# Kernel tuning notes

Hardware: AMD Instinct MI355X
Metric: run time of the kernel (lower is better)

## Reference

```python
import jax, jax.numpy as jnp
import numpy as np

HIDDEN = 4096
INTER = 14336
TOKENS = 4096


def setup_inputs() -> dict:
    key = jax.random.key(0)
    k_x, k_g, k_u, k_d = jax.random.split(key, 4)
    scale_in = 1.0 / np.sqrt(HIDDEN)
    scale_mid = 1.0 / np.sqrt(INTER)
    return {
        "x": jax.random.normal(k_x, (TOKENS, HIDDEN), dtype=jnp.float32),
        "w_gate": jax.random.normal(k_g, (HIDDEN, INTER), dtype=jnp.float32) * scale_in,
        "w_up": jax.random.normal(k_u, (HIDDEN, INTER), dtype=jnp.float32) * scale_in,
        "w_down": jax.random.normal(k_d, (INTER, HIDDEN), dtype=jnp.float32) * scale_mid,
    }


def reference(x, w_gate, w_up, w_down):
    # SwiGLU: down( silu(x @ Wg) * (x @ Wu) )
    gate = jax.nn.silu(jnp.einsum("td,df->tf", x, w_gate))  # [T, INTER]
    up = jnp.einsum("td,df->tf", x, w_up)                   # [T, INTER]
    return jnp.einsum("tf,fd->td", gate * up, w_down)       # [T, HIDDEN]
```

## Files before the change

### kernel.cpp

```cpp
#include <hip/hip_runtime.h>

#define H_DIM 4096
#define I_DIM 14336
#define T_DIM 4096
#define N2    (2*I_DIM)

typedef float  f32x4  __attribute__((ext_vector_type(4)));
typedef float  f32x2  __attribute__((ext_vector_type(2)));
typedef unsigned int u32x4 __attribute__((ext_vector_type(4)));
typedef unsigned int u32x2 __attribute__((ext_vector_type(2)));
typedef __bf16 bf16x8 __attribute__((ext_vector_type(8)));
typedef unsigned short u16;

__device__ __forceinline__ unsigned int pack2bf(float a, float b){
  unsigned int ua = __builtin_bit_cast(unsigned int, a);
  unsigned int ub = __builtin_bit_cast(unsigned int, b);
  ua = (ua + 0x7fffu + ((ua >> 16) & 1u)) >> 16;
  ub = (ub + 0x7fffu + ((ub >> 16) & 1u)) >> 16;
  return (ua & 0xffffu) | (ub << 16);
}
__device__ __forceinline__ u16 f2bf(float a){
  unsigned int u = __builtin_bit_cast(unsigned int, a);
  u = (u + 0x7fffu + ((u >> 16) & 1u)) >> 16;
  return (u16)u;
}
__device__ __forceinline__ bf16x8 lds_frag(const unsigned char* p){
  u32x4 v = *(const u32x4*)p;
  return __builtin_bit_cast(bf16x8, v);
}

#define GLOAD16(g, l) __builtin_amdgcn_global_load_lds( \
    (const __attribute__((address_space(1))) unsigned int*)(g), \
    (__attribute__((address_space(3))) unsigned int*)(l), 16, 0, 0)

#define WAITVM0  asm volatile("s_waitcnt vmcnt(0)" ::: "memory")
#define CFENCE   asm volatile("" ::: "memory")

__global__ __launch_bounds__(256)
void k_cast(const float* __restrict__ in, u16* __restrict__ out, long n)
{
  long i = ((long)blockIdx.x * 256 + threadIdx.x) * 8;
  if (i >= n) return;
  f32x4 a = *(const f32x4*)(in + i);
  f32x4 b = *(const f32x4*)(in + i + 4);
  u32x4 o = { pack2bf(a[0],a[1]), pack2bf(a[2],a[3]),
              pack2bf(b[0],b[1]), pack2bf(b[2],b[3]) };
  *(u32x4*)(out + i) = o;
}

__global__ __launch_bounds__(256)
void k_transpose(const float* __restrict__ in, u16* __restrict__ out,
                 int R, int C, int remap)
{
  __shared__ u16 tile[64][68];
  const int tid = threadIdx.x;
  const int r0 = blockIdx.x * 64, c0 = blockIdx.y * 64;
  const int lr  = tid >> 4;
  const int lc4 = (tid & 15) * 4;
  #pragma unroll
  for (int s = 0; s < 4; ++s){
    f32x4 v = *(const f32x4*)(in + (size_t)(r0 + lr + s*16) * C + c0 + lc4);
    #pragma unroll
    for (int j = 0; j < 4; ++j) tile[lc4 + j][lr + s*16] = f2bf(v[j]);
  }
  __syncthreads();
  #pragma unroll
  for (int s = 0; s < 4; ++s){
    int cl = lr + s*16;
    int n  = c0 + cl;
    int orow = (remap < 0) ? n : (((n >> 4) << 5) + (n & 15) + remap);
    u32x2 v = *(const u32x2*)&tile[cl][lc4];
    *(u32x2*)(out + (size_t)orow * R + r0 + lc4) = v;
  }
}

template<int EPI>
__global__ __launch_bounds__(512, 2)
void gemm9(const u16* __restrict__ A, const u16* __restrict__ B,
           void* __restrict__ Cout, const int K, const int ldc,
           const int mblocks)
{
  __shared__ unsigned char smem[131072];
  const int tid  = threadIdx.x;
  const int lane = tid & 63;
  const int wid  = tid >> 6;
  const int wm   = wid >> 2;
  const int wn   = wid & 3;

  const int nwg = gridDim.x;
  const int cpx = nwg >> 3;
  const int bid = blockIdx.x;
  const int swz = (bid & 7) * cpx + (bid >> 3);
  const int m0 = (swz % mblocks) << 8;
  const int n0 = (swz / mblocks) << 8;
  const int NT = K >> 6;

  const int srow = tid >> 3;
  const int gl   = (tid & 7) ^ (srow & 7);
  const u16* Ap = A + (size_t)(m0 + srow) * K + gl * 8;
  const u16* Bp = B + (size_t)(n0 + srow) * K + gl * 8;
  unsigned char* ldsw = smem + tid * 16;
  const size_t rowK64  = (size_t)64 * K;
  const size_t rowK128 = (size_t)128 * K;

  const int r15 = lane & 15;
  const int lhi = lane >> 4;
  const int gk0 = (((r15 >> 2) & 1) << 2) | (lhi ^ (r15 & 3));
  const int gk1 = gk0 ^ 4;
  const unsigned char* ldsr = smem + r15 * 128;

  f32x4 acc[8][4];
  #pragma unroll
  for (int i = 0; i < 8; ++i)
    #pragma unroll
    for (int j = 0; j < 4; ++j) acc[i][j] = (f32x4)0.0f;
  bf16x8 areg0[4][2], areg1[4][2];
  bf16x8 breg[2][2][2];

#define ISSUE(h) do { \
    const int _a = (h) & 3; \
    const size_t _k0 = (size_t)((h) >> 2) << 6; \
    unsigned char* _l = ldsw + (((h) & 7) << 14); \
    const u16* _s = (_a < 2 ? Bp + (size_t)_a * rowK128 \
                            : Ap + (size_t)(_a - 2) * rowK128) + _k0; \
    GLOAD16(_s, _l); \
    GLOAD16(_s + rowK64, _l + 8192); \
  } while (0)

#define RD_A(SLOT, MQ, DST) do { \
    const unsigned char* _b = ldsr + ((SLOT) << 14) + (MQ) * 8192; \
    _Pragma("unroll") \
    for (int _m = 0; _m < 4; ++_m) { \
      DST[_m][0] = lds_frag(_b + _m * 2048 + gk0 * 16); \
      DST[_m][1] = lds_frag(_b + _m * 2048 + gk1 * 16); \
    } \
  } while (0)

#define RD_B(SLOT, NQ) do { \
    const unsigned char* _b = ldsr + ((SLOT) << 14) + (wn & 1) * 8192 + (NQ) * 4096; \
    _Pragma("unroll") \
    for (int _n = 0; _n < 2; ++_n) { \
      breg[NQ][_n][0] = lds_frag(_b + _n * 2048 + gk0 * 16); \
      breg[NQ][_n][1] = lds_frag(_b + _n * 2048 + gk1 * 16); \
    } \
  } while (0)

#define MFMAQ(AR, MQ, NQ) \
    _Pragma("unroll") \
    for (int _m = 0; _m < 4; ++_m) \
      _Pragma("unroll") \
      for (int _n = 0; _n < 2; ++_n) { \
        acc[(MQ)*4+_m][(NQ)*2+_n] = __builtin_amdgcn_mfma_f32_16x16x32_bf16( \
            AR[_m][0], breg[NQ][_n][0], acc[(MQ)*4+_m][(NQ)*2+_n], 0, 0, 0); \
        acc[(MQ)*4+_m][(NQ)*2+_n] = __builtin_amdgcn_mfma_f32_16x16x32_bf16( \
            AR[_m][1], breg[NQ][_n][1], acc[(MQ)*4+_m][(NQ)*2+_n], 0, 0, 0); \
      }

  #pragma unroll
  for (int h = 0; h < 4; ++h) ISSUE(h);
  WAITVM0;
  __builtin_amdgcn_s_barrier();
  CFENCE;

  for (int t = 0; t < NT; ++t){
    const int bh = t << 2;
    const int sB = (bh + (wn >> 1)) & 7;
    const int sA = (bh + 2 + wm) & 7;
    const bool more = (t + 1 < NT);
    if (more){ ISSUE(bh + 4); ISSUE(bh + 5); ISSUE(bh + 6); ISSUE(bh + 7); }
    RD_A(sA, 0, areg0);
    RD_B(sB, 0);
    RD_B(sB, 1);
    MFMAQ(areg0, 0, 0);
    RD_A(sA, 1, areg1);
    MFMAQ(areg0, 0, 1);
    MFMAQ(areg1, 1, 1);
    MFMAQ(areg1, 1, 0);
    if (more) WAITVM0;
    __builtin_amdgcn_s_barrier();
    CFENCE;
  }

#undef ISSUE
#undef RD_A
#undef RD_B
#undef MFMAQ

  const int r0 = lhi * 4;
  if (EPI == 0){
    float* C = (float*)Cout;
    #pragma unroll
    for (int mi = 0; mi < 8; ++mi)
      #pragma unroll
      for (int nj = 0; nj < 4; ++nj)
        #pragma unroll
        for (int j = 0; j < 4; ++j)
          C[(size_t)(m0 + wm*128 + mi*16 + r0 + j) * ldc + n0 + wn*64 + nj*16 + r15] =
            acc[mi][nj][j];
  } else {
    u16* C = (u16*)Cout;
    const int hb = ((n0 + wn*64) >> 1);
    #pragma unroll
    for (int mi = 0; mi < 8; ++mi)
      #pragma unroll
      for (int p = 0; p < 2; ++p)
        #pragma unroll
        for (int j = 0; j < 4; ++j){
          float g = acc[mi][2*p][j];
          float u = acc[mi][2*p+1][j];
          float s = g / (1.0f + __expf(-g));
          C[(size_t)(m0 + wm*128 + mi*16 + r0 + j) * ldc + hb + p*16 + r15] =
            f2bf(s * u);
        }
  }
}

__global__ __launch_bounds__(256, 2)
void k_gateup_fb(const float* __restrict__ x, const float* __restrict__ wg,
                 const float* __restrict__ wu, u16* __restrict__ h)
{
  __shared__ unsigned char smem[61440];
  const int tid  = threadIdx.x;
  const int lane = tid & 63;
  const int wid  = tid >> 6;
  const int wr   = wid >> 1, wc = wid & 1;
  const int m0   = blockIdx.x * 128;
  const int n0   = blockIdx.y * 128;
  const int s_am = tid >> 3;
  const int s_ak = (tid & 7) * 4;
  const int s_bn = (tid & 63) * 2;
  const int s_bk = (tid >> 6) * 8;

  f32x4 accg[4][4], accu[4][4];
  #pragma unroll
  for (int i = 0; i < 4; ++i)
    #pragma unroll
    for (int j = 0; j < 4; ++j){ accg[i][j] = (f32x4)0.0f; accu[i][j] = (f32x4)0.0f; }

  f32x4 pa[4];
  f32x2 pg[8], pu[8];
  auto gload = [&](int kt){
    const int k0 = kt * 32;
    #pragma unroll
    for (int it = 0; it < 4; ++it)
      pa[it] = *(const f32x4*)(x + (size_t)(m0 + it*32 + s_am) * H_DIM + k0 + s_ak);
    #pragma unroll
    for (int r = 0; r < 8; ++r){
      pg[r] = *(const f32x2*)(wg + (size_t)(k0 + s_bk + r) * I_DIM + n0 + s_bn);
      pu[r] = *(const f32x2*)(wu + (size_t)(k0 + s_bk + r) * I_DIM + n0 + s_bn);
    }
  };
  auto sstore = [&](int b){
    unsigned char* Ab = smem + b * 10240;
    #pragma unroll
    for (int it = 0; it < 4; ++it){
      u32x2 v = { pack2bf(pa[it][0], pa[it][1]), pack2bf(pa[it][2], pa[it][3]) };
      *(u32x2*)(Ab + (s_am + it*32) * 80 + s_ak * 2) = v;
    }
    unsigned char* Bg = smem + 20480 + b * 10240;
    unsigned char* Bu = smem + 40960 + b * 10240;
    #pragma unroll
    for (int c = 0; c < 2; ++c){
      u32x4 vg = { pack2bf(pg[0][c], pg[1][c]), pack2bf(pg[2][c], pg[3][c]),
                   pack2bf(pg[4][c], pg[5][c]), pack2bf(pg[6][c], pg[7][c]) };
      *(u32x4*)(Bg + (s_bn + c) * 80 + s_bk * 2) = vg;
      u32x4 vu = { pack2bf(pu[0][c], pu[1][c]), pack2bf(pu[2][c], pu[3][c]),
                   pack2bf(pu[4][c], pu[5][c]), pack2bf(pu[6][c], pu[7][c]) };
      *(u32x4*)(Bu + (s_bn + c) * 80 + s_bk * 2) = vu;
    }
  };
  const int koff = (lane >> 4) * 16;
  const int ar   = wr * 64 + (lane & 15);
  const int br   = wc * 64 + (lane & 15);
  auto compute = [&](int b){
    const unsigned char* Ab = smem + b * 10240;
    const unsigned char* Bg = smem + 20480 + b * 10240;
    const unsigned char* Bu = smem + 40960 + b * 10240;
    bf16x8 a[4];
    #pragma unroll
    for (int mi = 0; mi < 4; ++mi)
      a[mi] = lds_frag(Ab + (ar + mi*16) * 80 + koff);
    #pragma unroll
    for (int nh = 0; nh < 2; ++nh){
      bf16x8 bg[2], bu[2];
      #pragma unroll
      for (int nj = 0; nj < 2; ++nj){
        bg[nj] = lds_frag(Bg + (br + (nh*2+nj)*16) * 80 + koff);
        bu[nj] = lds_frag(Bu + (br + (nh*2+nj)*16) * 80 + koff);
      }
      #pragma unroll
      for (int mi = 0; mi < 4; ++mi)
        #pragma unroll
        for (int nj = 0; nj < 2; ++nj){
          accg[mi][nh*2+nj] = __builtin_amdgcn_mfma_f32_16x16x32_bf16(a[mi], bg[nj], accg[mi][nh*2+nj], 0, 0, 0);
          accu[mi][nh*2+nj] = __builtin_amdgcn_mfma_f32_16x16x32_bf16(a[mi], bu[nj], accu[mi][nh*2+nj], 0, 0, 0);
        }
    }
  };
  gload(0); sstore(0); __syncthreads();
  const int NT = H_DIM / 32;
  for (int kt = 0; kt < NT; ++kt){
    const int b = kt & 1;
    if (kt + 1 < NT) gload(kt + 1);
    compute(b);
    if (kt + 1 < NT) sstore(b ^ 1);
    __syncthreads();
  }
  const int bm = wr * 64 + ((lane >> 4) << 2);
  const int bn = wc * 64 + (lane & 15);
  #pragma unroll
  for (int mi = 0; mi < 4; ++mi)
    #pragma unroll
    for (int ni = 0; ni < 4; ++ni)
      #pragma unroll
      for (int r = 0; r < 4; ++r){
        float gv = accg[mi][ni][r];
        float uv = accu[mi][ni][r];
        float s  = gv / (1.0f + __expf(-gv));
        h[(size_t)(m0 + bm + mi*16 + r) * I_DIM + n0 + bn + ni*16] = f2bf(s * uv);
      }
}

__global__ __launch_bounds__(256, 2)
void k_down_fb(const u16* __restrict__ h, const float* __restrict__ wd,
               float* __restrict__ out)
{
  __shared__ unsigned char smem[40960];
  const int tid  = threadIdx.x;
  const int lane = tid & 63;
  const int wid  = tid >> 6;
  const int wr   = wid >> 1, wc = wid & 1;
  const int m0   = blockIdx.x * 128;
  const int n0   = blockIdx.y * 128;
  const int s_am = tid >> 1;
  const int s_ak = (tid & 1) * 16;
  const int s_bn = (tid & 63) * 2;
  const int s_bk = (tid >> 6) * 8;

  f32x4 acc[4][4];
  #pragma unroll
  for (int i = 0; i < 4; ++i)
    #pragma unroll
    for (int j = 0; j < 4; ++j) acc[i][j] = (f32x4)0.0f;

  u32x4 pha[2];
  f32x2 pb[8];
  auto gload = [&](int kt){
    const int k0 = kt * 32;
    const u16* ap = h + (size_t)(m0 + s_am) * I_DIM + k0 + s_ak;
    pha[0] = *(const u32x4*)(ap);
    pha[1] = *(const u32x4*)(ap + 8);
    #pragma unroll
    for (int r = 0; r < 8; ++r)
      pb[r] = *(const f32x2*)(wd + (size_t)(k0 + s_bk + r) * H_DIM + n0 + s_bn);
  };
  auto sstore = [&](int b){
    unsigned char* Ab = smem + b * 10240;
    *(u32x4*)(Ab + s_am * 80 + s_ak * 2)      = pha[0];
    *(u32x4*)(Ab + s_am * 80 + s_ak * 2 + 16) = pha[1];
    unsigned char* Bb = smem + 20480 + b * 10240;
    #pragma unroll
    for (int c = 0; c < 2; ++c){
      u32x4 v = { pack2bf(pb[0][c], pb[1][c]), pack2bf(pb[2][c], pb[3][c]),
                  pack2bf(pb[4][c], pb[5][c]), pack2bf(pb[6][c], pb[7][c]) };
      *(u32x4*)(Bb + (s_bn + c) * 80 + s_bk * 2) = v;
    }
  };
  const int koff = (lane >> 4) * 16;
  const int ar   = wr * 64 + (lane & 15);
  const int br   = wc * 64 + (lane & 15);
  auto compute = [&](int b){
    const unsigned char* Ab = smem + b * 10240;
    const unsigned char* Bb = smem + 20480 + b * 10240;
    bf16x8 a[4];
    #pragma unroll
    for (int mi = 0; mi < 4; ++mi)
      a[mi] = lds_frag(Ab + (ar + mi*16) * 80 + koff);
    #pragma unroll
    for (int nh = 0; nh < 2; ++nh){
      bf16x8 bb[2];
      #pragma unroll
      for (int nj = 0; nj < 2; ++nj)
        bb[nj] = lds_frag(Bb + (br + (nh*2+nj)*16) * 80 + koff);
      #pragma unroll
      for (int mi = 0; mi < 4; ++mi)
        #pragma unroll
        for (int nj = 0; nj < 2; ++nj)
          acc[mi][nh*2+nj] = __builtin_amdgcn_mfma_f32_16x16x32_bf16(a[mi], bb[nj], acc[mi][nh*2+nj], 0, 0, 0);
    }
  };
  gload(0); sstore(0); __syncthreads();
  const int NT = I_DIM / 32;
  for (int kt = 0; kt < NT; ++kt){
    const int b = kt & 1;
    if (kt + 1 < NT) gload(kt + 1);
    compute(b);
    if (kt + 1 < NT) sstore(b ^ 1);
    __syncthreads();
  }
  const int bm = wr * 64 + ((lane >> 4) << 2);
  const int bn = wc * 64 + (lane & 15);
  #pragma unroll
  for (int mi = 0; mi < 4; ++mi)
    #pragma unroll
    for (int ni = 0; ni < 4; ++ni)
      #pragma unroll
      for (int r = 0; r < 4; ++r)
        out[(size_t)(m0 + bm + mi*16 + r) * H_DIM + n0 + bn + ni*16] = acc[mi][ni][r];
}

extern "C" void kernel_launch(void* const* d_in, const int* in_sizes, int n_in,
                              void* d_out, int out_size, void* d_ws, size_t ws_size,
                              hipStream_t stream)
{
  const float* x  = (const float*)d_in[0];
  const float* wg = (const float*)d_in[1];
  const float* wu = (const float*)d_in[2];
  const float* wd = (const float*)d_in[3];
  float* out = (float*)d_out;

  const size_t X_OFF   = 0;
  const size_t WGU_OFF = 33554432;
  const size_t WD_OFF  = 268435456;
  const size_t H_OFF   = 385875968;
  const size_t NEED    = 503316480;

  if (ws_size >= NEED){
    u16* xb  = (u16*)((char*)d_ws + X_OFF);
    u16* wgu = (u16*)((char*)d_ws + WGU_OFF);
    u16* wdt = (u16*)((char*)d_ws + WD_OFF);
    u16* h   = (u16*)((char*)d_ws + H_OFF);

    long nx = (long)T_DIM * H_DIM;
    k_cast<<<(unsigned)((nx/8 + 255)/256), 256, 0, stream>>>(x, xb, nx);
    dim3 tg(H_DIM/64, I_DIM/64);
    k_transpose<<<tg, 256, 0, stream>>>(wg, wgu, H_DIM, I_DIM, 0);
    k_transpose<<<tg, 256, 0, stream>>>(wu, wgu, H_DIM, I_DIM, 16);
    dim3 td(I_DIM/64, H_DIM/64);
    k_transpose<<<td, 256, 0, stream>>>(wd, wdt, I_DIM, H_DIM, -1);

    gemm9<1><<<dim3(16 * (N2/256)), dim3(512), 0, stream>>>(
        xb, wgu, h, H_DIM, I_DIM, T_DIM/256);
    gemm9<0><<<dim3(16 * (H_DIM/256)), dim3(512), 0, stream>>>(
        h, wdt, out, I_DIM, H_DIM, T_DIM/256);
  } else {
    u16* h = (u16*)d_ws;
    size_t maxrows = ws_size / ((size_t)I_DIM * 2);
    int chunk = (int)(maxrows > (size_t)T_DIM ? (size_t)T_DIM : maxrows);
    chunk &= ~127;
    if (chunk < 128) chunk = 128;
    for (int r0 = 0; r0 < T_DIM; r0 += chunk){
      int rows = (T_DIM - r0 < chunk) ? (T_DIM - r0) : chunk;
      dim3 g1(rows / 128, I_DIM / 128);
      dim3 g2(rows / 128, H_DIM / 128);
      k_gateup_fb<<<g1, dim3(256), 0, stream>>>(x + (size_t)r0 * H_DIM, wg, wu, h);
      k_down_fb  <<<g2, dim3(256), 0, stream>>>(h, wd, out + (size_t)r0 * H_DIM);
    }
  }
}
```

Measured before the change: 1.421 ms.

## Spread global-to-LDS prefetch across k-loop phases with finer barriers and priority

The GEMM main loop now issues one prefetch chunk per compute phase, staying six half-tiles ahead, instead of issuing four chunks at the top of each iteration and then waiting on all loads. It waits with vmcnt(4) instead of vmcnt(0) and adds a workgroup barrier between MFMA phases. MFMA sections are wrapped in s_setprio to favour the math waves. This is meant to keep loads in flight across iterations and hide memory latency, at the cost of three extra barriers per iteration and correctness depending on the ring-buffer slot reuse timing.

```diff
diff --git a/kernel.cpp b/kernel.cpp
--- a/kernel.cpp
+++ b/kernel.cpp
@@ -33,6 +33,7 @@
     (const __attribute__((address_space(1))) unsigned int*)(g), \
     (__attribute__((address_space(3))) unsigned int*)(l), 16, 0, 0)
 
+#define WAITVM4  asm volatile("s_waitcnt vmcnt(4)" ::: "memory")
 #define WAITVM0  asm volatile("s_waitcnt vmcnt(0)" ::: "memory")
 #define CFENCE   asm volatile("" ::: "memory")
 
@@ -76,9 +77,9 @@
 
 template<int EPI>
 __global__ __launch_bounds__(512, 2)
-void gemm9(const u16* __restrict__ A, const u16* __restrict__ B,
-           void* __restrict__ Cout, const int K, const int ldc,
-           const int mblocks)
+void gemm10(const u16* __restrict__ A, const u16* __restrict__ B,
+            void* __restrict__ Cout, const int K, const int ldc,
+            const int mblocks)
 {
   __shared__ unsigned char smem[131072];
   const int tid  = threadIdx.x;
@@ -157,8 +158,8 @@
       }
 
   #pragma unroll
-  for (int h = 0; h < 4; ++h) ISSUE(h);
-  WAITVM0;
+  for (int h = 0; h < 6; ++h) ISSUE(h);
+  WAITVM4;
   __builtin_amdgcn_s_barrier();
   CFENCE;
 
@@ -166,17 +167,34 @@
     const int bh = t << 2;
     const int sB = (bh + (wn >> 1)) & 7;
     const int sA = (bh + 2 + wm) & 7;
-    const bool more = (t + 1 < NT);
-    if (more){ ISSUE(bh + 4); ISSUE(bh + 5); ISSUE(bh + 6); ISSUE(bh + 7); }
+    const int lim = NT << 2;
     RD_A(sA, 0, areg0);
     RD_B(sB, 0);
+    if (bh + 6 < lim) ISSUE(bh + 6);
+    __builtin_amdgcn_s_setprio(1);
+    MFMAQ(areg0, 0, 0);
+    __builtin_amdgcn_s_setprio(0);
+    __builtin_amdgcn_s_barrier();
+    CFENCE;
     RD_B(sB, 1);
-    MFMAQ(areg0, 0, 0);
+    if (bh + 7 < lim) ISSUE(bh + 7);
+    __builtin_amdgcn_s_setprio(1);
+    MFMAQ(areg0, 0, 1);
+    __builtin_amdgcn_s_setprio(0);
+    __builtin_amdgcn_s_barrier();
+    CFENCE;
     RD_A(sA, 1, areg1);
-    MFMAQ(areg0, 0, 1);
+    if (bh + 8 < lim) ISSUE(bh + 8);
+    __builtin_amdgcn_s_setprio(1);
     MFMAQ(areg1, 1, 1);
+    __builtin_amdgcn_s_setprio(0);
+    __builtin_amdgcn_s_barrier();
+    CFENCE;
+    if (bh + 9 < lim) ISSUE(bh + 9);
+    __builtin_amdgcn_s_setprio(1);
     MFMAQ(areg1, 1, 0);
-    if (more) WAITVM0;
+    __builtin_amdgcn_s_setprio(0);
+    if (t + 2 < NT) { WAITVM4; } else { WAITVM0; }
     __builtin_amdgcn_s_barrier();
     CFENCE;
   }
@@ -439,9 +457,9 @@
     dim3 td(I_DIM/64, H_DIM/64);
     k_transpose<<<td, 256, 0, stream>>>(wd, wdt, I_DIM, H_DIM, -1);
 
-    gemm9<1><<<dim3(16 * (N2/256)), dim3(512), 0, stream>>>(
+    gemm10<1><<<dim3(16 * (N2/256)), dim3(512), 0, stream>>>(
         xb, wgu, h, H_DIM, I_DIM, T_DIM/256);
-    gemm9<0><<<dim3(16 * (H_DIM/256)), dim3(512), 0, stream>>>(
+    gemm10<0><<<dim3(16 * (H_DIM/256)), dim3(512), 0, stream>>>(
         h, wdt, out, I_DIM, H_DIM, T_DIM/256);
   } else {
     u16* h = (u16*)d_ws;
```

After: 1.431 ms. No clear change (+0.7%).
